# Performance work log

Measured on AMD Instinct MI355X. Metric: run time of the kernel, lower is better.

Reference implementation:

```python
import jax, jax.numpy as jnp
import numpy as np
import math

B, S, E, H = 2, 2048, 2048, 16
HD = E // H // 2  # 64, per-head dim of each differential half
DEPTH = 12
LAMBDA_INIT = 0.8 - 0.6 * math.exp(-0.3 * DEPTH)
EPS = 1e-5


def setup_inputs() -> dict:
    key = jax.random.key(0)
    ks = jax.random.split(key, 10)
    sc = 0.02
    return {
        "x": jax.random.normal(ks[0], (B, S, E), jnp.float32),
        "Wq": jax.random.normal(ks[1], (E, E), jnp.float32) * sc,
        "Wk": jax.random.normal(ks[2], (E, E), jnp.float32) * sc,
        "Wv": jax.random.normal(ks[3], (E, E), jnp.float32) * sc,
        "Wo": jax.random.normal(ks[4], (E, E), jnp.float32) * sc,
        "lambda_q1": jax.random.normal(ks[5], (HD,), jnp.float32) * 0.1,
        "lambda_k1": jax.random.normal(ks[6], (HD,), jnp.float32) * 0.1,
        "lambda_q2": jax.random.normal(ks[7], (HD,), jnp.float32) * 0.1,
        "lambda_k2": jax.random.normal(ks[8], (HD,), jnp.float32) * 0.1,
        "gamma": jnp.ones((2 * HD,), jnp.float32),
    }


def _rope_interleaved(x, cos, sin):
    # x: [b, s, h, d]; cos/sin: [s, d//2]; pairs are (0,1),(2,3),...
    xe, xo = x[..., 0::2], x[..., 1::2]
    c = cos[None, :, None, :]
    s = sin[None, :, None, :]
    oe = xe * c - xo * s
    oo = xe * s + xo * c
    return jnp.stack([oe, oo], axis=-1).reshape(x.shape)


def reference(x, Wq, Wk, Wv, Wo, lambda_q1, lambda_k1, lambda_q2, lambda_k2, gamma):
    b, t, _ = x.shape
    # rotary tables (rotary dim == HD, interleaved)
    angle = 1.0 / 10000 ** jnp.linspace(0.0, 1.0, HD // 2, dtype=jnp.float32)
    freqs = jnp.arange(t, dtype=jnp.float32)[:, None] * angle  # [t, HD//2]
    cos, sin = jnp.cos(freqs), jnp.sin(freqs)

    q = (x @ Wq.T).reshape(b, t, 2 * H, HD)
    k = (x @ Wk.T).reshape(b, t, 2 * H, HD)
    v = (x @ Wv.T).reshape(b, t, H, 2 * HD)  # concat(v1, v2) along last dim

    q = _rope_interleaved(q, cos, sin)
    k = _rope_interleaved(k, cos, sin)

    q = q.reshape(b, t, H, 2, HD)
    k = k.reshape(b, t, H, 2, HD)
    q1, q2 = q[:, :, :, 0], q[:, :, :, 1]
    k1, k2 = k[:, :, :, 0], k[:, :, :, 1]

    scale = HD ** -0.5  # flash_attn default softmax scale
    # branch 1: softmax(q1 k1) @ [v1|v2]
    s1 = jnp.einsum("bthd,bshd->bhts", q1, k1) * scale
    p1 = jax.nn.softmax(s1, axis=-1)
    o1 = jnp.einsum("bhts,bshd->bthd", p1, v)  # [b,t,H,2*HD]
    # branch 2: softmax(q2 k2) @ [v1|v2]
    s2 = jnp.einsum("bthd,bshd->bhts", q2, k2) * scale
    p2 = jax.nn.softmax(s2, axis=-1)
    o2 = jnp.einsum("bhts,bshd->bthd", p2, v)

    lam1 = jnp.exp(jnp.sum(lambda_q1 * lambda_k1))
    lam2 = jnp.exp(jnp.sum(lambda_q2 * lambda_k2))
    lam = lam1 - lam2 + LAMBDA_INIT

    attn = o1 - lam * o2  # [b,t,H,2*HD]
    # RMSNorm over last dim (2*HD) with affine gamma
    rms = jax.lax.rsqrt(jnp.mean(attn * attn, axis=-1, keepdims=True) + EPS)
    attn = attn * rms * gamma
    attn = attn * (1.0 - LAMBDA_INIT)
    attn = attn.reshape(b, t, H * 2 * HD)
    return attn @ Wo.T
```

## Files before the change

### kernel.cpp

```cpp
#include <hip/hip_runtime.h>
#include <cstdint>
#include <cstddef>

typedef unsigned short u16;
typedef __attribute__((ext_vector_type(8))) short short8;
typedef __attribute__((ext_vector_type(4))) float f32x4;
typedef __attribute__((ext_vector_type(16))) float f32x16;

#define MFMA_B16(a,b,c) __builtin_amdgcn_mfma_f32_16x16x32_bf16((a),(b),(c),0,0,0)
#define MFMA32(a,b,c)  __builtin_amdgcn_mfma_f32_32x32x16_bf16((a),(b),(c),0,0,0)

#define S_LEN 2048
#define EMB 2048
#define QKV_N 6144
#define HD 64
#define LAMBDA_INIT_F 0.78360576653162f
#define ONE_MINUS_LI 0.21639423346838f
#define EXP2_SCALE 0.18033688011112042f

static __device__ __forceinline__ u16 f2bf(float f) {
  unsigned u = __float_as_uint(f);
  unsigned r = ((u >> 16) & 1u) + 0x7fffu;
  return (u16)((u + r) >> 16);
}
static __device__ __forceinline__ float bf2f(u16 h) {
  return __uint_as_float(((unsigned)h) << 16);
}
static __device__ __forceinline__ unsigned cvt_pk_bf16(float lo, float hi) {
  unsigned r;
  asm("v_cvt_pk_bf16_f32 %0, %1, %2" : "=v"(r) : "v"(lo), "v"(hi));
  return r;
}
static __device__ __forceinline__ void gload_lds16(const u16* g, u16* l) {
  __builtin_amdgcn_global_load_lds((const __attribute__((address_space(1))) void*)g,
                                   (__attribute__((address_space(3))) void*)l, 16, 0, 0);
}

__global__ void cvt_f32_bf16(const float* __restrict__ s, u16* __restrict__ d, int n4) {
  int i = blockIdx.x * 256 + threadIdx.x;
  if (i >= n4) return;
  f32x4 v = *(const f32x4*)&s[i * 4];
  unsigned lo = cvt_pk_bf16(v[0], v[1]);
  unsigned hi = cvt_pk_bf16(v[2], v[3]);
  *(unsigned long long*)&d[i * 4] = (unsigned long long)lo | ((unsigned long long)hi << 32);
}

template <int BF16OUT>
__global__ __launch_bounds__(256, 2) void gemm_bt(const u16* __restrict__ A,
                                                  const u16* __restrict__ B,
                                                  void* __restrict__ Cout,
                                                  int M, int N, int K) {
  __shared__ u16 As[128 * 32];
  __shared__ u16 Bs[128 * 32];
  const int tid = threadIdx.x;
  const int lane = tid & 63, wv = tid >> 6;
  const int bm = blockIdx.x * 128, bn = blockIdx.y * 128;
  const int wr = (wv >> 1) * 64, wc = (wv & 1) * 64;
  const int lr = lane & 15, hk = lane >> 4;

  const int r0 = tid >> 2;
  const int c0 = (tid & 3) * 8;
  const u16* ga = A + (size_t)(bm + r0) * K + c0;
  const u16* gb = B + (size_t)(bn + r0) * K + c0;
  const size_t rstep = (size_t)64 * K;

  f32x4 acc[4][4] = {};

  for (int k0 = 0; k0 < K; k0 += 32) {
    __syncthreads();
    gload_lds16(ga + k0,         &As[(tid) * 8]);
    gload_lds16(ga + rstep + k0, &As[(tid + 256) * 8]);
    gload_lds16(gb + k0,         &Bs[(tid) * 8]);
    gload_lds16(gb + rstep + k0, &Bs[(tid + 256) * 8]);
    __syncthreads();
    short8 af[4], bfv[4];
#pragma unroll
    for (int i = 0; i < 4; i++) af[i] = *(const short8*)&As[(wr + i * 16 + lr) * 32 + hk * 8];
#pragma unroll
    for (int j = 0; j < 4; j++) bfv[j] = *(const short8*)&Bs[(wc + j * 16 + lr) * 32 + hk * 8];
#pragma unroll
    for (int i = 0; i < 4; i++)
#pragma unroll
      for (int j = 0; j < 4; j++)
        acc[i][j] = MFMA_B16(af[i], bfv[j], acc[i][j]);
  }

  if (BF16OUT) {
    u16* C = (u16*)Cout;
#pragma unroll
    for (int i = 0; i < 4; i++)
#pragma unroll
      for (int j = 0; j < 4; j++)
#pragma unroll
        for (int r = 0; r < 4; r++) {
          int row = bm + wr + i * 16 + hk * 4 + r;
          int col = bn + wc + j * 16 + lr;
          C[(size_t)row * N + col] = f2bf(acc[i][j][r]);
        }
  } else {
    float* C = (float*)Cout;
#pragma unroll
    for (int i = 0; i < 4; i++)
#pragma unroll
      for (int j = 0; j < 4; j++)
#pragma unroll
        for (int r = 0; r < 4; r++) {
          int row = bm + wr + i * 16 + hk * 4 + r;
          int col = bn + wc + j * 16 + lr;
          C[(size_t)row * N + col] = acc[i][j][r];
        }
  }
}

__global__ void rope_kernel(u16* __restrict__ qkv) {
  int idx = blockIdx.x * 256 + threadIdx.x;
  int p = idx & 31;
  int u = (idx >> 5) & 63;
  int m = idx >> 11;
  int t = m & (S_LEN - 1);
  int col = (u < 32) ? (u * 64 + 2 * p) : (EMB + (u - 32) * 64 + 2 * p);
  u16* ptr = qkv + (size_t)m * QKV_N + col;
  unsigned v = *(unsigned*)ptr;
  float xe = bf2f((u16)(v & 0xffff));
  float xo = bf2f((u16)(v >> 16));
  float w = expf((float)p * (-9.210340371976184f / 31.0f));
  float ang = (float)t * w;
  float sn, cs;
  sincosf(ang, &sn, &cs);
  float oe = xe * cs - xo * sn;
  float oo = xe * sn + xo * cs;
  *(unsigned*)ptr = (unsigned)f2bf(oe) | (((unsigned)f2bf(oo)) << 16);
}

#define SW(row, colByte) ((((row)) << 7) + ((colByte) ^ (((row) & 7) << 4)))

#define QKT(Kc, Q0, Q1, Q2, Q3, KT, Pc, LSUM)                                    \
  do {                                                                           \
    f32x16 s = {};                                                               \
    s = MFMA32(*(const short8*)((Kc) + SW((KT) * 32 + l31, 0  + hi16)), Q0, s);  \
    s = MFMA32(*(const short8*)((Kc) + SW((KT) * 32 + l31, 32 + hi16)), Q1, s);  \
    s = MFMA32(*(const short8*)((Kc) + SW((KT) * 32 + l31, 64 + hi16)), Q2, s);  \
    s = MFMA32(*(const short8*)((Kc) + SW((KT) * 32 + l31, 96 + hi16)), Q3, s);  \
    _Pragma("unroll") for (int r = 0; r < 16; r += 4) {                          \
      float e0 = __builtin_amdgcn_exp2f(s[r]     * EXP2_SCALE);                  \
      float e1 = __builtin_amdgcn_exp2f(s[r + 1] * EXP2_SCALE);                  \
      float e2 = __builtin_amdgcn_exp2f(s[r + 2] * EXP2_SCALE);                  \
      float e3 = __builtin_amdgcn_exp2f(s[r + 3] * EXP2_SCALE);                  \
      LSUM += (e0 + e1) + (e2 + e3);                                             \
      unsigned lo_ = cvt_pk_bf16(e0, e1);                                        \
      unsigned hi_ = cvt_pk_bf16(e2, e3);                                        \
      *(unsigned long long*)((Pc) + SW(l31, (KT) * 64 + (r >> 2) * 16 + hi8)) =  \
          (unsigned long long)lo_ | ((unsigned long long)hi_ << 32);             \
    }                                                                            \
  } while (0)

#define PVD(DT, O1, O2)                                                          \
  do {                                                                           \
    short8 va0 = *(const short8*)(VTc + SW((DT) * 32 + l31, 0  + hi16));         \
    short8 va1 = *(const short8*)(VTc + SW((DT) * 32 + l31, 32 + hi16));         \
    short8 va2 = *(const short8*)(VTc + SW((DT) * 32 + l31, 64 + hi16));         \
    short8 va3 = *(const short8*)(VTc + SW((DT) * 32 + l31, 96 + hi16));         \
    O1 = MFMA32(va0, p1f0, O1); O1 = MFMA32(va1, p1f1, O1);                      \
    O1 = MFMA32(va2, p1f2, O1); O1 = MFMA32(va3, p1f3, O1);                      \
    O2 = MFMA32(va0, p2f0, O2); O2 = MFMA32(va1, p2f1, O2);                      \
    O2 = MFMA32(va2, p2f2, O2); O2 = MFMA32(va3, p2f3, O2);                      \
  } while (0)

__global__ __launch_bounds__(256, 2) void attn_kernel(
    const u16* __restrict__ qkv, u16* __restrict__ attnb,
    const float* __restrict__ lq1, const float* __restrict__ lk1,
    const float* __restrict__ lq2, const float* __restrict__ lk2,
    const float* __restrict__ gamma) {
  __shared__ u16 K1s[64 * 64];
  __shared__ u16 K2s[64 * 64];
  __shared__ u16 VTs[128 * 64];
  __shared__ u16 Ps[4 * 2 * 32 * 64];

  const int g = blockIdx.x;
  const int xcd = g & 7;
  const int gi = g >> 3;
  const int bh = xcd * 4 + (gi >> 4);
  const int qt = gi & 15;
  const int b = bh >> 4, h = bh & 15;

  const int tid = threadIdx.x, lane = tid & 63, wv = tid >> 6;
  const int l31 = lane & 31;
  const int hi16 = (lane >> 5) * 16;
  const int hi8 = (lane >> 5) * 8;
  const int hi4 = (lane >> 5) * 4;

  float d1 = lq1[lane] * lk1[lane];
  float d2 = lq2[lane] * lk2[lane];
#pragma unroll
  for (int off = 32; off; off >>= 1) { d1 += __shfl_xor(d1, off); d2 += __shfl_xor(d2, off); }
  const float lam = __expf(d1) - __expf(d2) + LAMBDA_INIT_F;

  const int qbase = qt * 128 + wv * 32;
  const u16* qp1 = qkv + (size_t)(b * S_LEN + qbase + l31) * QKV_N + (2 * h) * 64;
  const u16* qp2 = qp1 + 64;
  short8 q1f0 = *(const short8*)(qp1 + hi8);
  short8 q1f1 = *(const short8*)(qp1 + 16 + hi8);
  short8 q1f2 = *(const short8*)(qp1 + 32 + hi8);
  short8 q1f3 = *(const short8*)(qp1 + 48 + hi8);
  short8 q2f0 = *(const short8*)(qp2 + hi8);
  short8 q2f1 = *(const short8*)(qp2 + 16 + hi8);
  short8 q2f2 = *(const short8*)(qp2 + 32 + hi8);
  short8 q2f3 = *(const short8*)(qp2 + 48 + hi8);

  f32x16 o1t0 = {}, o1t1 = {}, o1t2 = {}, o1t3 = {};
  f32x16 o2t0 = {}, o2t1 = {}, o2t2 = {}, o2t3 = {};
  float l1p = 0.f, l2p = 0.f;

  const int gl_row = wv * 8 + (lane >> 3);
  const int gl_cb  = ((lane & 7) ^ (lane >> 3)) * 8;
  u16* k1d = &K1s[(wv * 8) * 64 + lane * 8];
  u16* k2d = &K2s[(wv * 8) * 64 + lane * 8];

  const int vkv = (tid & 31) * 2;
  const int vd0 = (tid >> 5) * 8;

  const u16* kb1 = qkv + (size_t)b * S_LEN * QKV_N + EMB + (2 * h) * 64;
  const u16* kb2 = kb1 + 64;
  const u16* vbp = qkv + (size_t)b * S_LEN * QKV_N + 2 * EMB + h * 128;

  char* K1c = (char*)K1s;
  char* K2c = (char*)K2s;
  char* VTc = (char*)VTs;
  char* P1c = (char*)&Ps[(wv * 2 + 0) * 32 * 64];
  char* P2c = (char*)&Ps[(wv * 2 + 1) * 32 * 64];

  for (int kv0 = 0; kv0 < S_LEN; kv0 += 64) {
    __syncthreads();
    {
      const u16* g1 = kb1 + (size_t)(kv0 + gl_row) * QKV_N + gl_cb;
      const u16* g2 = kb2 + (size_t)(kv0 + gl_row) * QKV_N + gl_cb;
      gload_lds16(g1, k1d);
      gload_lds16(g1 + (size_t)32 * QKV_N, k1d + 32 * 64);
      gload_lds16(g2, k2d);
      gload_lds16(g2 + (size_t)32 * QKV_N, k2d + 32 * 64);
    }
    {
      const u16* vs = vbp + (size_t)(kv0 + vkv) * QKV_N + vd0;
      short8 a0 = *(const short8*)vs;
      short8 a1 = *(const short8*)(vs + QKV_N);
      short8 b0 = *(const short8*)(vs + 64);
      short8 b1 = *(const short8*)(vs + QKV_N + 64);
#pragma unroll
      for (int j = 0; j < 8; j++) {
        unsigned pk0 = (unsigned)(u16)a0[j] | (((unsigned)(u16)a1[j]) << 16);
        *(unsigned*)(VTc + SW(vd0 + j, vkv * 2)) = pk0;
        unsigned pk1 = (unsigned)(u16)b0[j] | (((unsigned)(u16)b1[j]) << 16);
        *(unsigned*)(VTc + SW(vd0 + 64 + j, vkv * 2)) = pk1;
      }
    }
    __syncthreads();

    QKT(K1c, q1f0, q1f1, q1f2, q1f3, 0, P1c, l1p);
    QKT(K1c, q1f0, q1f1, q1f2, q1f3, 1, P1c, l1p);
    QKT(K2c, q2f0, q2f1, q2f2, q2f3, 0, P2c, l2p);
    QKT(K2c, q2f0, q2f1, q2f2, q2f3, 1, P2c, l2p);
    asm volatile("" ::: "memory");

    short8 p1f0 = *(const short8*)(P1c + SW(l31, 0  + hi16));
    short8 p1f1 = *(const short8*)(P1c + SW(l31, 32 + hi16));
    short8 p1f2 = *(const short8*)(P1c + SW(l31, 64 + hi16));
    short8 p1f3 = *(const short8*)(P1c + SW(l31, 96 + hi16));
    short8 p2f0 = *(const short8*)(P2c + SW(l31, 0  + hi16));
    short8 p2f1 = *(const short8*)(P2c + SW(l31, 32 + hi16));
    short8 p2f2 = *(const short8*)(P2c + SW(l31, 64 + hi16));
    short8 p2f3 = *(const short8*)(P2c + SW(l31, 96 + hi16));

    PVD(0, o1t0, o2t0);
    PVD(1, o1t1, o2t1);
    PVD(2, o1t2, o2t2);
    PVD(3, o1t3, o2t3);
    asm volatile("" ::: "memory");
  }

  float l1 = l1p + __shfl_xor(l1p, 32);
  float l2 = l2p + __shfl_xor(l2p, 32);
  const float inv1 = 1.f / l1;
  const float inv2 = 1.f / l2;

  float ss = 0.f;
#define COMB(O1, O2)                                                   \
  _Pragma("unroll") for (int i = 0; i < 16; i++) {                     \
    float a = O1[i] * inv1 - lam * (O2[i] * inv2);                     \
    O1[i] = a;                                                         \
    ss += a * a;                                                       \
  }
  COMB(o1t0, o2t0) COMB(o1t1, o2t1) COMB(o1t2, o2t2) COMB(o1t3, o2t3)
#undef COMB
  ss += __shfl_xor(ss, 32);
  const float sc2 = rsqrtf(ss * (1.f / 128.f) + 1e-5f) * ONE_MINUS_LI;

  u16* orow = attnb + (size_t)(b * S_LEN + qbase + l31) * EMB + h * 128;
#define WRT(O1, T)                                                              \
  _Pragma("unroll") for (int gg = 0; gg < 4; gg++) {                            \
    int d = (T) * 32 + gg * 8 + hi4;                                            \
    f32x4 gv = *(const f32x4*)&gamma[d];                                        \
    unsigned wlo = cvt_pk_bf16(O1[4 * gg] * gv[0] * sc2, O1[4 * gg + 1] * gv[1] * sc2); \
    unsigned whi = cvt_pk_bf16(O1[4 * gg + 2] * gv[2] * sc2, O1[4 * gg + 3] * gv[3] * sc2); \
    *(unsigned long long*)&orow[d] = (unsigned long long)wlo | ((unsigned long long)whi << 32); \
  }
  WRT(o1t0, 0) WRT(o1t1, 1) WRT(o1t2, 2) WRT(o1t3, 3)
#undef WRT
}

extern "C" void kernel_launch(void* const* d_in, const int* in_sizes, int n_in,
                              void* d_out, int out_size, void* d_ws, size_t ws_size,
                              hipStream_t stream) {
  (void)in_sizes; (void)n_in; (void)out_size; (void)ws_size;
  const float* x   = (const float*)d_in[0];
  const float* Wq  = (const float*)d_in[1];
  const float* Wk  = (const float*)d_in[2];
  const float* Wv  = (const float*)d_in[3];
  const float* Wo  = (const float*)d_in[4];
  const float* lq1 = (const float*)d_in[5];
  const float* lk1 = (const float*)d_in[6];
  const float* lq2 = (const float*)d_in[7];
  const float* lk2 = (const float*)d_in[8];
  const float* gam = (const float*)d_in[9];

  char* ws = (char*)d_ws;
  u16* xb    = (u16*)(ws);
  u16* Wcat  = (u16*)(ws + 16777216);
  u16* Wob   = (u16*)(ws + 41943040);
  u16* qkv   = (u16*)(ws + 50331648);
  u16* attnb = xb;

  const int NE = EMB * EMB;
  cvt_f32_bf16<<<(2 * NE / 4 + 255) / 256, 256, 0, stream>>>(x, xb, 2 * NE / 4);
  cvt_f32_bf16<<<(NE / 4 + 255) / 256, 256, 0, stream>>>(Wq, Wcat, NE / 4);
  cvt_f32_bf16<<<(NE / 4 + 255) / 256, 256, 0, stream>>>(Wk, Wcat + NE, NE / 4);
  cvt_f32_bf16<<<(NE / 4 + 255) / 256, 256, 0, stream>>>(Wv, Wcat + 2 * NE, NE / 4);
  cvt_f32_bf16<<<(NE / 4 + 255) / 256, 256, 0, stream>>>(Wo, Wob, NE / 4);

  dim3 g1(4096 / 128, QKV_N / 128);
  gemm_bt<1><<<g1, 256, 0, stream>>>(xb, Wcat, qkv, 4096, QKV_N, EMB);

  rope_kernel<<<(4096 * 64 * 32) / 256, 256, 0, stream>>>(qkv);

  attn_kernel<<<512, 256, 0, stream>>>(qkv, attnb, lq1, lk1, lq2, lk2, gam);

  dim3 g2(4096 / 128, EMB / 128);
  gemm_bt<0><<<g2, 256, 0, stream>>>(attnb, Wob, d_out, 4096, EMB, EMB);
}
```

Baseline: 375.2 us.

## Split attention work across wave pairs over KV columns and head dims

Each block now handles 64 query rows instead of 128. Two waves share one 32-row query group: each computes half of the KV columns for QK^T and half of the 128 output dims for PV, and partial softmax row sums and RMS sums are combined through shared memory. This doubles the grid to 1024 blocks and halves the accumulator registers per wave, to raise occupancy and parallelism. The cost is an extra __syncthreads per KV step, twice as many K/V tile loads overall across blocks, and cross-wave reductions at the end.

```diff
diff --git a/kernel.cpp b/kernel.cpp
--- a/kernel.cpp
+++ b/kernel.cpp
@@ -174,16 +174,20 @@
   __shared__ u16 K1s[64 * 64];
   __shared__ u16 K2s[64 * 64];
   __shared__ u16 VTs[128 * 64];
-  __shared__ u16 Ps[4 * 2 * 32 * 64];
+  __shared__ u16 Ps[2 * 2 * 32 * 64];
+  __shared__ float Lr[2][2][2][32];
+  __shared__ float Sr[2][2][32];
 
   const int g = blockIdx.x;
   const int xcd = g & 7;
   const int gi = g >> 3;
-  const int bh = xcd * 4 + (gi >> 4);
-  const int qt = gi & 15;
+  const int bh = xcd * 4 + (gi >> 5);
+  const int qt = gi & 31;
   const int b = bh >> 4, h = bh & 15;
 
   const int tid = threadIdx.x, lane = tid & 63, wv = tid >> 6;
+  const int qg = wv >> 1;
+  const int dh = wv & 1;
   const int l31 = lane & 31;
   const int hi16 = (lane >> 5) * 16;
   const int hi8 = (lane >> 5) * 8;
@@ -195,7 +199,7 @@
   for (int off = 32; off; off >>= 1) { d1 += __shfl_xor(d1, off); d2 += __shfl_xor(d2, off); }
   const float lam = __expf(d1) - __expf(d2) + LAMBDA_INIT_F;
 
-  const int qbase = qt * 128 + wv * 32;
+  const int qbase = qt * 64 + qg * 32;
   const u16* qp1 = qkv + (size_t)(b * S_LEN + qbase + l31) * QKV_N + (2 * h) * 64;
   const u16* qp2 = qp1 + 64;
   short8 q1f0 = *(const short8*)(qp1 + hi8);
@@ -207,8 +211,7 @@
   short8 q2f2 = *(const short8*)(qp2 + 32 + hi8);
   short8 q2f3 = *(const short8*)(qp2 + 48 + hi8);
 
-  f32x16 o1t0 = {}, o1t1 = {}, o1t2 = {}, o1t3 = {};
-  f32x16 o2t0 = {}, o2t1 = {}, o2t2 = {}, o2t3 = {};
+  f32x16 o1t0 = {}, o1t1 = {}, o2t0 = {}, o2t1 = {};
   float l1p = 0.f, l2p = 0.f;
 
   const int gl_row = wv * 8 + (lane >> 3);
@@ -226,8 +229,8 @@
   char* K1c = (char*)K1s;
   char* K2c = (char*)K2s;
   char* VTc = (char*)VTs;
-  char* P1c = (char*)&Ps[(wv * 2 + 0) * 32 * 64];
-  char* P2c = (char*)&Ps[(wv * 2 + 1) * 32 * 64];
+  char* P1c = (char*)&Ps[(qg * 2 + 0) * 32 * 64];
+  char* P2c = (char*)&Ps[(qg * 2 + 1) * 32 * 64];
 
   for (int kv0 = 0; kv0 < S_LEN; kv0 += 64) {
     __syncthreads();
@@ -255,11 +258,9 @@
     }
     __syncthreads();
 
-    QKT(K1c, q1f0, q1f1, q1f2, q1f3, 0, P1c, l1p);
-    QKT(K1c, q1f0, q1f1, q1f2, q1f3, 1, P1c, l1p);
-    QKT(K2c, q2f0, q2f1, q2f2, q2f3, 0, P2c, l2p);
-    QKT(K2c, q2f0, q2f1, q2f2, q2f3, 1, P2c, l2p);
-    asm volatile("" ::: "memory");
+    QKT(K1c, q1f0, q1f1, q1f2, q1f3, dh, P1c, l1p);
+    QKT(K2c, q2f0, q2f1, q2f2, q2f3, dh, P2c, l2p);
+    __syncthreads();
 
     short8 p1f0 = *(const short8*)(P1c + SW(l31, 0  + hi16));
     short8 p1f1 = *(const short8*)(P1c + SW(l31, 32 + hi16));
@@ -270,17 +271,16 @@
     short8 p2f2 = *(const short8*)(P2c + SW(l31, 64 + hi16));
     short8 p2f3 = *(const short8*)(P2c + SW(l31, 96 + hi16));
 
-    PVD(0, o1t0, o2t0);
-    PVD(1, o1t1, o2t1);
-    PVD(2, o1t2, o2t2);
-    PVD(3, o1t3, o2t3);
-    asm volatile("" ::: "memory");
+    PVD(dh * 2 + 0, o1t0, o2t0);
+    PVD(dh * 2 + 1, o1t1, o2t1);
   }
 
   float l1 = l1p + __shfl_xor(l1p, 32);
   float l2 = l2p + __shfl_xor(l2p, 32);
-  const float inv1 = 1.f / l1;
-  const float inv2 = 1.f / l2;
+  if (lane < 32) { Lr[qg][0][dh][l31] = l1; Lr[qg][1][dh][l31] = l2; }
+  __syncthreads();
+  const float inv1 = 1.f / (Lr[qg][0][0][l31] + Lr[qg][0][1][l31]);
+  const float inv2 = 1.f / (Lr[qg][1][0][l31] + Lr[qg][1][1][l31]);
 
   float ss = 0.f;
 #define COMB(O1, O2)                                                   \
@@ -289,21 +289,24 @@
     O1[i] = a;                                                         \
     ss += a * a;                                                       \
   }
-  COMB(o1t0, o2t0) COMB(o1t1, o2t1) COMB(o1t2, o2t2) COMB(o1t3, o2t3)
+  COMB(o1t0, o2t0) COMB(o1t1, o2t1)
 #undef COMB
   ss += __shfl_xor(ss, 32);
-  const float sc2 = rsqrtf(ss * (1.f / 128.f) + 1e-5f) * ONE_MINUS_LI;
+  if (lane < 32) Sr[qg][dh][l31] = ss;
+  __syncthreads();
+  const float SS = Sr[qg][0][l31] + Sr[qg][1][l31];
+  const float sc2 = rsqrtf(SS * (1.f / 128.f) + 1e-5f) * ONE_MINUS_LI;
 
   u16* orow = attnb + (size_t)(b * S_LEN + qbase + l31) * EMB + h * 128;
-#define WRT(O1, T)                                                              \
+#define WRT(O1, DT)                                                             \
   _Pragma("unroll") for (int gg = 0; gg < 4; gg++) {                            \
-    int d = (T) * 32 + gg * 8 + hi4;                                            \
+    int d = dh * 64 + (DT) * 32 + gg * 8 + hi4;                                 \
     f32x4 gv = *(const f32x4*)&gamma[d];                                        \
     unsigned wlo = cvt_pk_bf16(O1[4 * gg] * gv[0] * sc2, O1[4 * gg + 1] * gv[1] * sc2); \
     unsigned whi = cvt_pk_bf16(O1[4 * gg + 2] * gv[2] * sc2, O1[4 * gg + 3] * gv[3] * sc2); \
     *(unsigned long long*)&orow[d] = (unsigned long long)wlo | ((unsigned long long)whi << 32); \
   }
-  WRT(o1t0, 0) WRT(o1t1, 1) WRT(o1t2, 2) WRT(o1t3, 3)
+  WRT(o1t0, 0) WRT(o1t1, 1)
 #undef WRT
 }
 
@@ -341,7 +344,7 @@
 
   rope_kernel<<<(4096 * 64 * 32) / 256, 256, 0, stream>>>(qkv);
 
-  attn_kernel<<<512, 256, 0, stream>>>(qkv, attnb, lq1, lk1, lq2, lk2, gam);
+  attn_kernel<<<1024, 256, 0, stream>>>(qkv, attnb, lq1, lk1, lq2, lk2, gam);
 
   dim3 g2(4096 / 128, EMB / 128);
   gemm_bt<0><<<g2, 256, 0, stream>>>(attnb, Wob, d_out, 4096, EMB, EMB);
```

After: 355.5 us. -5.3%, faster.
